# Optimization experiments

Measured on AMD Instinct MI355X. Metric: run time of the kernel, lower is better.

The kernel has to match this reference:

```python
import jax, jax.numpy as jnp
import numpy as np

N_QUBITS = 10
N_QLAYERS = 4
INV_SQRT2 = 1.0 / np.sqrt(2.0)


def setup_inputs() -> dict:
    key = jax.random.key(0)
    k1, k2 = jax.random.split(key)
    x = jax.random.normal(k1, (16, 256, 2 * N_QUBITS), dtype=jnp.float32)
    weights = jax.random.uniform(k2, (N_QLAYERS, N_QUBITS, 3), dtype=jnp.float32,
                                 minval=-np.pi, maxval=np.pi)
    return {"x": x, "weights": weights}


def _ry_mat(t):
    # t: scalar or (B,) -> (...,2,2) complex64 rotation about Y
    c = jnp.cos(t * 0.5)
    s = jnp.sin(t * 0.5)
    row0 = jnp.stack([c, -s], axis=-1)
    row1 = jnp.stack([s, c], axis=-1)
    return jnp.stack([row0, row1], axis=-2).astype(jnp.complex64)


def _rz_mat(p):
    # t: scalar or (B,) -> (...,2,2) complex64 diag(e^{-ip/2}, e^{+ip/2})
    e = jnp.exp(-0.5j * p.astype(jnp.complex64))
    z = jnp.zeros_like(e)
    row0 = jnp.stack([e, z], axis=-1)
    row1 = jnp.stack([z, jnp.conj(e)], axis=-1)
    return jnp.stack([row0, row1], axis=-2)


def _apply_1q(state, U, wire):
    # state: (B, 2,...,2); U: (2,2) shared or (B,2,2) per-sample
    ax = wire + 1
    s = jnp.moveaxis(state, ax, -1)
    if U.ndim == 3:
        s = jnp.einsum('bij,b...j->b...i', U, s)
    else:
        s = jnp.einsum('ij,...j->...i', U, s)
    return jnp.moveaxis(s, -1, ax)


def _apply_cnot(state, ctrl, tgt):
    a, b = ctrl + 1, tgt + 1
    s0 = jax.lax.index_in_dim(state, 0, axis=a, keepdims=True)
    s1 = jax.lax.index_in_dim(state, 1, axis=a, keepdims=True)
    s1 = jnp.flip(s1, axis=b)  # X on target within control=1 block
    return jnp.concatenate([s0, s1], axis=a)


def _circuit(x_flat, weights):
    n = N_QUBITS
    Bf = x_flat.shape[0]
    theta = jnp.pi * (x_flat[:, :n] + 1.0) * 0.5
    phi = jnp.pi * (x_flat[:, n:2 * n] + 1.0) * 0.5
    H = jnp.array([[1.0, 1.0], [1.0, -1.0]], dtype=jnp.complex64) * INV_SQRT2

    # |0...0> batched statevector: (Bf, 2, ..., 2)
    state = jnp.zeros((Bf, 2 ** n), dtype=jnp.complex64).at[:, 0].set(1.0)
    state = state.reshape((Bf,) + (2,) * n)

    # encoding layer
    for i in range(n):
        state = _apply_1q(state, H, i)
        state = _apply_1q(state, _ry_mat(theta[:, i]), i)
        state = _apply_1q(state, _rz_mat(phi[:, i]), i)

    # variational layers
    for layer in range(N_QLAYERS):
        for i in range(n):
            state = _apply_1q(state, _rz_mat(weights[layer, i, 0]), i)
            state = _apply_1q(state, _ry_mat(weights[layer, i, 1]), i)
            state = _apply_1q(state, _rz_mat(weights[layer, i, 2]), i)
        off = 1 if layer % 2 == 0 else n // 2
        for i in range(n):
            state = _apply_cnot(state, i, (i + off) % n)

    # <Z_i> = sum |amp|^2 * (+1 if qubit i = 0 else -1)
    probs = state.real ** 2 + state.imag ** 2
    zs = []
    for i in range(n):
        p = jnp.moveaxis(probs, i + 1, -1).reshape(Bf, -1, 2)
        zs.append(p[..., 0].sum(-1) - p[..., 1].sum(-1))
    return jnp.stack(zs, axis=-1)  # (Bf, n_qubits)


def reference(x, weights):
    B, L, _ = x.shape
    out = _circuit(x.reshape(-1, 2 * N_QUBITS), weights)
    return out.reshape(B, L, N_QUBITS)
```

## Files before the change

kernel.cpp:

```cpp
#include <hip/hip_runtime.h>
#include <math.h>

#define NQ 10
#define NLAYERS 4
#define NGATES (NLAYERS * NQ)

typedef float v2f __attribute__((ext_vector_type(2)));
typedef float v4f __attribute__((ext_vector_type(4)));

__device__ __forceinline__ v2f mk2(float a, float b) { v2f r; r.x = a; r.y = b; return r; }

__device__ __forceinline__ v2f cmul_m(v4f m, v2f s) {
    v2f r = m.xy * s;
    return __builtin_elementwise_fma(m.zw, s.yx, r);
}
__device__ __forceinline__ v2f cfma_m(v2f acc, v4f m, v2f s) {
    acc = __builtin_elementwise_fma(m.xy, s, acc);
    acc = __builtin_elementwise_fma(m.zw, s.yx, acc);
    return acc;
}
__device__ __forceinline__ v2f cmul(v2f a, v2f b) {
    v2f r = a.xx * b;
    return __builtin_elementwise_fma(mk2(-a.y, a.y), b.yx, r);
}
__device__ __forceinline__ v4f pack_u(float re, float im) {
    v4f m; m.x = re; m.y = re; m.z = -im; m.w = im; return m;
}

__host__ __device__ constexpr int pxor1(int v) {
    int y = v; y ^= y >> 1; y ^= y >> 2; y ^= y >> 4; y ^= y >> 8;
    return (y & 0x1FF) | (((y ^ (v >> 9)) & 1) << 9);
}
__host__ __device__ constexpr int pxor5(int v) {
    int lo = v & 31, hi = (v >> 5) & 31;
    return (lo << 5) | (lo ^ hi);
}

__device__ __forceinline__ void apply_gate(v2f* st, const v4f* __restrict__ M, int b) {
    v4f m0 = M[0], m1 = M[1], m2 = M[2], m3 = M[3];
    #pragma unroll
    for (int g = 0; g < 16; ++g) {
        int r0 = ((g >> b) << (b + 1)) | (g & ((1 << b) - 1));
        int r1 = r0 | (1 << b);
        v2f s0v = st[r0], s1v = st[r1];
        v2f n0 = cmul_m(m0, s0v); n0 = cfma_m(n0, m1, s1v);
        v2f n1 = cmul_m(m2, s0v); n1 = cfma_m(n1, m3, s1v);
        st[r0] = n0; st[r1] = n1;
    }
}

__device__ __forceinline__ void load_contig(v2f* st, const v2f* scratch, int lane) {
    const v4f* rp = (const v4f*)(scratch + 34 * lane);
    #pragma unroll
    for (int k = 0; k < 16; ++k) { v4f t = rp[k]; st[2 * k] = t.xy; st[2 * k + 1] = t.zw; }
}

__global__ __launch_bounds__(64) void qsim_kernel(const float* __restrict__ x,
                                                  const float* __restrict__ w,
                                                  float* __restrict__ out)
{
    __shared__ __align__(16) v2f scratch[2176];
    __shared__ __align__(16) v4f matsL[NGATES * 4];
    __shared__ __align__(16) v2f encf[2][NQ][2];

    const int lane = threadIdx.x;
    const int s = lane >> 5, sl = lane & 31;
    const long sample = 2L * blockIdx.x + s;

    if (lane < NGATES) {
        float w0 = w[lane * 3 + 0], w1 = w[lane * 3 + 1], w2 = w[lane * 3 + 2];
        float hs = 0.5f * (w0 + w2), hd = 0.5f * (w0 - w2), hy = 0.5f * w1;
        float cy, sy, cs, ss, cd, sd;
        sincosf(hy, &sy, &cy);
        sincosf(hs, &ss, &cs);
        sincosf(hd, &sd, &cd);
        matsL[lane * 4 + 0] = pack_u( cy * cs, -cy * ss);
        matsL[lane * 4 + 1] = pack_u(-sy * cd, -sy * sd);
        matsL[lane * 4 + 2] = pack_u( sy * cd, -sy * sd);
        matsL[lane * 4 + 3] = pack_u( cy * cs,  cy * ss);
    }
    __syncthreads();

    if (sl < NQ) {
        const float* xs = x + sample * (2 * NQ);
        float th = 0.7853981633974483f * (xs[sl] + 1.0f);
        float ph = 0.7853981633974483f * (xs[NQ + sl] + 1.0f);
        float cy, sy, cp, sp;
        sincosf(th, &sy, &cy);
        sincosf(ph, &sp, &cp);
        const float inv = 0.7071067811865476f;
        float a = (cy - sy) * inv, b = (cy + sy) * inv;
        v2f f0 = mk2(cp * a, -sp * a);
        v2f f1 = mk2(cp * b,  sp * b);
        v4f M0 = matsL[sl * 4 + 0], M1 = matsL[sl * 4 + 1];
        v4f M2 = matsL[sl * 4 + 2], M3 = matsL[sl * 4 + 3];
        encf[s][sl][0] = cfma_m(cmul_m(M0, f0), M1, f1);
        encf[s][sl][1] = cfma_m(cmul_m(M2, f0), M3, f1);
    }
    __syncthreads();

    v2f st[32];
    {
        v2f P = encf[s][5][(sl >> 4) & 1];
        P = cmul(P, encf[s][6][(sl >> 3) & 1]);
        P = cmul(P, encf[s][7][(sl >> 2) & 1]);
        P = cmul(P, encf[s][8][(sl >> 1) & 1]);
        P = cmul(P, encf[s][9][sl & 1]);
        v2f q01[4], q23[4], q234[8], Pq[4];
        #pragma unroll
        for (int a2 = 0; a2 < 4; ++a2) {
            q01[a2] = cmul(encf[s][0][(a2 >> 1) & 1], encf[s][1][a2 & 1]);
            q23[a2] = cmul(encf[s][2][(a2 >> 1) & 1], encf[s][3][a2 & 1]);
        }
        #pragma unroll
        for (int b2 = 0; b2 < 8; ++b2)
            q234[b2] = cmul(q23[b2 >> 1], encf[s][4][b2 & 1]);
        #pragma unroll
        for (int a2 = 0; a2 < 4; ++a2) Pq[a2] = cmul(P, q01[a2]);
        #pragma unroll
        for (int r = 0; r < 32; ++r)
            st[r] = cmul(Pq[r >> 3], q234[r & 7]);
    }

    const int jb1 = pxor1(sl), jb5 = pxor5(sl);

    #pragma unroll
    for (int r = 0; r < 32; ++r) {
        const int j = pxor1(r << 5) ^ jb1;
        scratch[1088 * s + 34 * (j >> 5) + (j & 31)] = st[r];
    }
    __syncthreads();
    load_contig(st, scratch, lane);

    #pragma unroll
    for (int l = 1; l < NLAYERS; ++l) {
        #pragma unroll
        for (int q = 5; q <= 9; ++q)
            apply_gate(st, matsL + (l * NQ + q) * 4, 9 - q);

        __syncthreads();
        {
            v2f* wp = scratch + 1088 * s + sl;
            #pragma unroll
            for (int r = 0; r < 32; ++r) wp[34 * r] = st[r];
        }
        __syncthreads();
        load_contig(st, scratch, lane);

        #pragma unroll
        for (int q = 0; q <= 4; ++q)
            apply_gate(st, matsL + (l * NQ + q) * 4, 4 - q);

        if (l < NLAYERS - 1) {
            __syncthreads();
            #pragma unroll
            for (int r = 0; r < 32; ++r) {
                const int jc = (l & 1) ? pxor5(r << 5) : pxor1(r << 5);
                const int j = jc ^ ((l & 1) ? jb5 : jb1);
                scratch[1088 * s + 34 * (j >> 5) + (j & 31)] = st[r];
            }
            __syncthreads();
            load_contig(st, scratch, lane);
        }
    }

    {
        float p[32];
        #pragma unroll
        for (int r = 0; r < 32; ++r) {
            v2f a = st[r];
            v2f sq = a * a;
            p[r] = sq.x + sq.y;
        }
        float t0 = 0.f, t1 = 0.f, t2 = 0.f, t3 = 0.f, t4 = 0.f;
        float s0a[16], s1a[8], s2a[4], s3a[2];
        #pragma unroll
        for (int k = 0; k < 16; ++k) { s0a[k] = p[2*k] + p[2*k+1]; t0 += p[2*k] - p[2*k+1]; }
        #pragma unroll
        for (int k = 0; k < 8; ++k)  { s1a[k] = s0a[2*k] + s0a[2*k+1]; t1 += s0a[2*k] - s0a[2*k+1]; }
        #pragma unroll
        for (int k = 0; k < 4; ++k)  { s2a[k] = s1a[2*k] + s1a[2*k+1]; t2 += s1a[2*k] - s1a[2*k+1]; }
        #pragma unroll
        for (int k = 0; k < 2; ++k)  { s3a[k] = s2a[2*k] + s2a[2*k+1]; t3 += s2a[2*k] - s2a[2*k+1]; }
        float S = s3a[0] + s3a[1];   t4 = s3a[0] - s3a[1];

        float acc[NQ];
        #pragma unroll
        for (int q = 0; q < 5; ++q)
            acc[q] = ((sl >> (4 - q)) & 1) ? -S : S;
        acc[5] = ((sl >> 4) & 1) ? -t4 : t4;
        acc[6] = ((sl >> 3) & 1) ? -t3 : t3;
        acc[7] = ((sl >> 2) & 1) ? -t2 : t2;
        acc[8] = ((sl >> 1) & 1) ? -t1 : t1;
        acc[9] = (sl & 1)        ? -t0 : t0;

        #pragma unroll
        for (int q = 0; q < NQ; ++q) {
            #pragma unroll
            for (int o = 16; o >= 1; o >>= 1)
                acc[q] += __shfl_xor(acc[q], o);
        }
        float v = acc[0];
        #pragma unroll
        for (int q = 1; q < NQ; ++q) v = (sl == q) ? acc[q] : v;
        if (sl < NQ)
            out[sample * NQ + sl] = v;
    }
}

extern "C" void kernel_launch(void* const* d_in, const int* in_sizes, int n_in,
                              void* d_out, int out_size, void* d_ws, size_t ws_size,
                              hipStream_t stream) {
    const float* x = (const float*)d_in[0];
    const float* w = (const float*)d_in[1];
    float* out = (float*)d_out;
    const int n_samples = in_sizes[0] / (2 * NQ);
    qsim_kernel<<<n_samples / 2, 64, 0, stream>>>(x, w, out);
}
```

Baseline: 78.55 us.

## Build post-CNOT encoded state directly in registers and pad scratch rows to 33

The initial product state is now built directly in the permuted (post-first-CNOT-layer) layout by indexing the per-qubit encoding factors with XOR-combined bits. This removes one shared-memory scatter, a barrier and a gather. It also changes the scratch row stride from 34 to 33 complex values to avoid bank conflicts, at the cost of replacing 16-byte vector loads with 8-byte loads.

```diff
diff --git a/kernel.cpp b/kernel.cpp
--- a/kernel.cpp
+++ b/kernel.cpp
@@ -49,17 +49,17 @@
     }
 }
 
-__device__ __forceinline__ void load_contig(v2f* st, const v2f* scratch, int lane) {
-    const v4f* rp = (const v4f*)(scratch + 34 * lane);
+__device__ __forceinline__ void load_row(v2f* st, const v2f* scratch, int lane) {
+    const v2f* rp = scratch + 33 * lane;
     #pragma unroll
-    for (int k = 0; k < 16; ++k) { v4f t = rp[k]; st[2 * k] = t.xy; st[2 * k + 1] = t.zw; }
+    for (int k = 0; k < 32; ++k) st[k] = rp[k];
 }
 
 __global__ __launch_bounds__(64) void qsim_kernel(const float* __restrict__ x,
                                                   const float* __restrict__ w,
                                                   float* __restrict__ out)
 {
-    __shared__ __align__(16) v2f scratch[2176];
+    __shared__ __align__(16) v2f scratch[2112];
     __shared__ __align__(16) v4f matsL[NGATES * 4];
     __shared__ __align__(16) v2f encf[2][NQ][2];
 
@@ -101,36 +101,34 @@
 
     v2f st[32];
     {
-        v2f P = encf[s][5][(sl >> 4) & 1];
-        P = cmul(P, encf[s][6][(sl >> 3) & 1]);
-        P = cmul(P, encf[s][7][(sl >> 2) & 1]);
-        P = cmul(P, encf[s][8][(sl >> 1) & 1]);
-        P = cmul(P, encf[s][9][sl & 1]);
-        v2f q01[4], q23[4], q234[8], Pq[4];
-        #pragma unroll
-        for (int a2 = 0; a2 < 4; ++a2) {
-            q01[a2] = cmul(encf[s][0][(a2 >> 1) & 1], encf[s][1][a2 & 1]);
-            q23[a2] = cmul(encf[s][2][(a2 >> 1) & 1], encf[s][3][a2 & 1]);
-        }
-        #pragma unroll
-        for (int b2 = 0; b2 < 8; ++b2)
-            q234[b2] = cmul(q23[b2 >> 1], encf[s][4][b2 & 1]);
-        #pragma unroll
-        for (int a2 = 0; a2 < 4; ++a2) Pq[a2] = cmul(P, q01[a2]);
-        #pragma unroll
-        for (int r = 0; r < 32; ++r)
-            st[r] = cmul(Pq[r >> 3], q234[r & 7]);
+        const int s0 = sl & 1, s1 = (sl >> 1) & 1, s2 = (sl >> 2) & 1,
+                  s3 = (sl >> 3) & 1, s4 = (sl >> 4) & 1;
+        v2f L = cmul(encf[s][2][s2 ^ s3], encf[s][3][s1 ^ s2]);
+        L = cmul(L, encf[s][4][s0 ^ s1]);
+        v2f A0 = cmul(encf[s][0][s4],     encf[s][1][s3 ^ s4]);
+        v2f A1 = cmul(encf[s][0][1 ^ s4], encf[s][1][1 ^ s3 ^ s4]);
+        v2f LA0 = cmul(L, A0), LA1 = cmul(L, A1);
+        v2f G0 = encf[s][5][s0], G1 = encf[s][5][1 ^ s0];
+        v2f D[2][2];
+        D[0][0] = cmul(LA0, G0); D[0][1] = cmul(LA0, G1);
+        D[1][0] = cmul(LA1, G0); D[1][1] = cmul(LA1, G1);
+        v2f C98[2][2], C76[2][2];
+        #pragma unroll
+        for (int a2 = 0; a2 < 2; ++a2)
+            #pragma unroll
+            for (int b2 = 0; b2 < 2; ++b2) {
+                C98[a2][b2] = cmul(encf[s][9][a2], encf[s][8][b2]);
+                C76[a2][b2] = cmul(encf[s][7][a2], encf[s][6][b2]);
+            }
+        #pragma unroll
+        for (int r = 0; r < 32; ++r) {
+            const int r0 = r & 1, r1 = (r >> 1) & 1, r2 = (r >> 2) & 1,
+                      r3 = (r >> 3) & 1, r4 = (r >> 4) & 1;
+            st[r] = cmul(cmul(D[r0][r4], C98[r0 ^ r1][r1 ^ r2]), C76[r2 ^ r3][r3 ^ r4]);
+        }
     }
 
     const int jb1 = pxor1(sl), jb5 = pxor5(sl);
-
-    #pragma unroll
-    for (int r = 0; r < 32; ++r) {
-        const int j = pxor1(r << 5) ^ jb1;
-        scratch[1088 * s + 34 * (j >> 5) + (j & 31)] = st[r];
-    }
-    __syncthreads();
-    load_contig(st, scratch, lane);
 
     #pragma unroll
     for (int l = 1; l < NLAYERS; ++l) {
@@ -140,12 +138,12 @@
 
         __syncthreads();
         {
-            v2f* wp = scratch + 1088 * s + sl;
-            #pragma unroll
-            for (int r = 0; r < 32; ++r) wp[34 * r] = st[r];
+            v2f* wp = scratch + 1056 * s + sl;
+            #pragma unroll
+            for (int r = 0; r < 32; ++r) wp[33 * r] = st[r];
         }
         __syncthreads();
-        load_contig(st, scratch, lane);
+        load_row(st, scratch, lane);
 
         #pragma unroll
         for (int q = 0; q <= 4; ++q)
@@ -157,10 +155,10 @@
             for (int r = 0; r < 32; ++r) {
                 const int jc = (l & 1) ? pxor5(r << 5) : pxor1(r << 5);
                 const int j = jc ^ ((l & 1) ? jb5 : jb1);
-                scratch[1088 * s + 34 * (j >> 5) + (j & 31)] = st[r];
+                scratch[1056 * s + 33 * (j >> 5) + (j & 31)] = st[r];
             }
             __syncthreads();
-            load_contig(st, scratch, lane);
+            load_row(st, scratch, lane);
         }
     }
 
```

Result: no change. 79.30 us (+0.9%).
